# Performance work log

Hardware: AMD Instinct MI355X
Metric: run time of the kernel (lower is better)

The kernel has to match this reference:

```python
import jax, jax.numpy as jnp
import numpy as np
import math

EMBED_DIM = 768
NUM_FRAMES = 48
NUM_FREQS = 10
C_IN = 3
FOURIER_DIM = 4 * NUM_FREQS  # include_uv=False
PM_HID = C_IN * 9 * 4        # patch_mlp_ratio=4
OM_HID = EMBED_DIM * 4       # out_mlp_ratio=4
B, N, T, H, W = 4, 8192, 48, 256, 256


def setup_inputs() -> dict:
    key = jax.random.key(0)
    ks = jax.random.split(key, 16)
    uv = jax.random.uniform(ks[0], (B, N, 2), dtype=jnp.float32)
    ts = jax.random.randint(ks[1], (B, N, 3), 0, NUM_FRAMES).astype(jnp.float32)
    query = jnp.concatenate([uv, ts], axis=-1)  # (B,N,5)
    images = jax.random.normal(ks[2], (B, C_IN, T, H, W), dtype=jnp.float32)
    def xavier(k, fan_in, fan_out):
        lim = math.sqrt(6.0 / (fan_in + fan_out))
        return jax.random.uniform(k, (fan_in, fan_out), dtype=jnp.float32, minval=-lim, maxval=lim)
    return {
        "query": query,
        "images": images,
        "uv_w": xavier(ks[3], FOURIER_DIM, EMBED_DIM),
        "uv_b": jnp.zeros((EMBED_DIM,), jnp.float32),
        "t_src_emb": 0.02 * jax.random.normal(ks[4], (NUM_FRAMES, EMBED_DIM), dtype=jnp.float32),
        "t_tgt_emb": 0.02 * jax.random.normal(ks[5], (NUM_FRAMES, EMBED_DIM), dtype=jnp.float32),
        "t_cam_emb": 0.02 * jax.random.normal(ks[6], (NUM_FRAMES, EMBED_DIM), dtype=jnp.float32),
        "pm_w1": xavier(ks[7], C_IN * 9, PM_HID),
        "pm_b1": jnp.zeros((PM_HID,), jnp.float32),
        "pm_w2": xavier(ks[8], PM_HID, EMBED_DIM),
        "pm_b2": jnp.zeros((EMBED_DIM,), jnp.float32),
        "om_w1": xavier(ks[9], EMBED_DIM, OM_HID),
        "om_b1": jnp.zeros((OM_HID,), jnp.float32),
        "om_w2": xavier(ks[10], OM_HID, EMBED_DIM),
        "om_b2": jnp.zeros((EMBED_DIM,), jnp.float32),
    }


def reference(query, images, uv_w, uv_b, t_src_emb, t_tgt_emb, t_cam_emb,
              pm_w1, pm_b1, pm_w2, pm_b2, om_w1, om_b1, om_w2, om_b2):
    # images: (B,C,T,H,W) -> (B,T,C,H,W)
    images = jnp.transpose(images, (0, 2, 1, 3, 4))
    Bq, Nq, _ = query.shape
    _, Tq, C, Hh, Ww = images.shape

    uv = jnp.clip(query[..., 0:2].astype(jnp.float32), 0.0, 1.0)  # (B,N,2)
    t_src = jnp.clip(jnp.round(query[..., 2]).astype(jnp.int32), 0, NUM_FRAMES - 1)
    t_tgt = jnp.clip(jnp.round(query[..., 3]).astype(jnp.int32), 0, NUM_FRAMES - 1)
    t_cam = jnp.clip(jnp.round(query[..., 4]).astype(jnp.int32), 0, NUM_FRAMES - 1)

    # Fourier features of (u,v)
    fb = 2.0 ** jnp.arange(NUM_FREQS, dtype=jnp.float32)  # (F,)
    u = uv[..., 0:1]
    v = uv[..., 1:2]
    up = (2.0 * math.pi) * u * fb  # (B,N,F)
    vp = (2.0 * math.pi) * v * fb
    feat = jnp.concatenate([jnp.sin(up), jnp.cos(up), jnp.sin(vp), jnp.cos(vp)], axis=-1)

    token1 = feat @ uv_w + uv_b              # (B,N,D)
    token2 = t_src_emb[t_src]                # embedding lookups
    token3 = t_tgt_emb[t_tgt]
    token4 = t_cam_emb[t_cam]

    # 3x3 patch gather centered at discrete (u,v) pixel of frame t_src
    x = jnp.round(uv[..., 0] * (Ww - 1)).astype(jnp.int32)  # (B,N)
    y = jnp.round(uv[..., 1] * (Hh - 1)).astype(jnp.int32)
    d = jnp.arange(-1, 2, dtype=jnp.int32)
    x_idx = jnp.clip(x[..., None] + d, 0, Ww - 1)  # (B,N,3)
    y_idx = jnp.clip(y[..., None] + d, 0, Hh - 1)  # (B,N,3)
    b_idx = jnp.arange(Bq)[:, None, None, None, None]
    c_idx = jnp.arange(C)[:, None, None]
    # direct fancy-index gather -> (B,N,C,3,3); avoids materializing (B,N,C,H,W)
    patches = images[b_idx,
                     t_src[:, :, None, None, None],
                     c_idx,
                     y_idx[:, :, None, :, None],
                     x_idx[:, :, None, None, :]]
    patch_flat = patches.reshape(Bq, Nq, C * 9)

    h = jax.nn.gelu(patch_flat @ pm_w1 + pm_b1, approximate=False)
    token5 = h @ pm_w2 + pm_b2

    out = token1 + token2 + token3 + token4 + token5
    out = jax.nn.gelu(out @ om_w1 + om_b1, approximate=False) @ om_w2 + om_b2
    return out
```

## Files before the change

### kernel.cpp

```cpp
#include <hip/hip_runtime.h>

typedef __bf16 bf16x8 __attribute__((ext_vector_type(8)));
typedef float  f32x4  __attribute__((ext_vector_type(4)));

#define GAS(p) ((const __attribute__((address_space(1))) void*)(p))
#define LAS(p) ((__attribute__((address_space(3))) void*)(p))
#define VMCNT(n) asm volatile("s_waitcnt vmcnt(" #n ")" ::: "memory")

__device__ __forceinline__ float gelu_exact(float x) {
    return 0.5f * x * (1.f + erff(x * 0.70710678118654752440f));
}

enum { EPI_X = 0, EPI_GELU = 1, EPI_OUT = 2 };

__global__ __launch_bounds__(256) void stage1_kernel(
    const float* __restrict__ query, const float* __restrict__ images,
    const float* __restrict__ pm_w1, const float* __restrict__ pm_b1,
    __bf16* __restrict__ G, int* __restrict__ tbuf)
{
    __shared__ float patch[4][28];
    const int wave = threadIdx.x >> 6, lane = threadIdx.x & 63;
    const int p = blockIdx.x * 4 + wave;
    const float* q = query + (size_t)p * 5;
    float u = fminf(fmaxf(q[0], 0.f), 1.f);
    float v = fminf(fmaxf(q[1], 0.f), 1.f);
    int ts = min(max((int)rintf(q[2]), 0), 47);
    int tt = min(max((int)rintf(q[3]), 0), 47);
    int tc = min(max((int)rintf(q[4]), 0), 47);
    const int b = p >> 13;
    if (lane < 27) {
        int c = lane / 9, rem = lane % 9, dy = rem / 3, dx = rem % 3;
        int x = (int)rintf(u * 255.f), y = (int)rintf(v * 255.f);
        int xx = min(max(x + dx - 1, 0), 255);
        int yy = min(max(y + dy - 1, 0), 255);
        size_t idx = ((size_t)((b * 3 + c) * 48 + ts) << 16) + ((size_t)yy << 8) + (size_t)xx;
        patch[wave][lane] = images[idx];
    }
    if (lane < 40) {
        int i = lane % 10;
        float base = (lane < 20) ? u : v;
        float ph = 6.28318530717958647693f * base * exp2f((float)i);
        float val = ((lane / 10) & 1) ? cosf(ph) : sinf(ph);
        G[(size_t)p * 192 + lane] = (__bf16)val;
    }
    for (int j = 148 + lane; j < 192; j += 64) G[(size_t)p * 192 + j] = (__bf16)0.f;
    if (lane < 3) tbuf[p * 3 + lane] = (lane == 0) ? ts : (lane == 1) ? tt : tc;
    __syncthreads();
    for (int j = lane; j < 108; j += 64) {
        float acc = pm_b1[j];
        #pragma unroll
        for (int i2 = 0; i2 < 27; i2++)
            acc = fmaf(patch[wave][i2], pm_w1[i2 * 108 + j], acc);
        G[(size_t)p * 192 + 40 + j] = (__bf16)gelu_exact(acc);
    }
}

__global__ __launch_bounds__(256) void transpose_to_bf16(
    const float* __restrict__ src, __bf16* __restrict__ dst, int R, int C)
{
    __shared__ float t[32][33];
    const int c0 = blockIdx.x * 32, r0 = blockIdx.y * 32;
    const int tx = threadIdx.x & 31, ty = threadIdx.x >> 5;
    #pragma unroll
    for (int i = 0; i < 32; i += 8)
        t[ty + i][tx] = src[(size_t)(r0 + ty + i) * C + (c0 + tx)];
    __syncthreads();
    #pragma unroll
    for (int i = 0; i < 32; i += 8)
        dst[(size_t)(c0 + ty + i) * R + (r0 + tx)] = (__bf16)t[tx][ty + i];
}

__global__ __launch_bounds__(256) void build_wcat(
    const float* __restrict__ uv_w, const float* __restrict__ pm_w2, __bf16* __restrict__ Wt)
{
    int idx = blockIdx.x * 256 + threadIdx.x;
    int n = idx / 192, k = idx % 192;
    float v = 0.f;
    if (k < 40) v = uv_w[k * 768 + n];
    else if (k < 148) v = pm_w2[(k - 40) * 768 + n];
    Wt[idx] = (__bf16)v;
}

template <int EPI, typename OutT>
__global__ __launch_bounds__(256) void gemm_bt(
    const __bf16* __restrict__ A, const __bf16* __restrict__ Bt, int K,
    const float* __restrict__ bias, const float* __restrict__ bias2,
    const int* __restrict__ tbuf,
    const float* __restrict__ e0, const float* __restrict__ e1, const float* __restrict__ e2,
    OutT* __restrict__ Cmat, int N)
{
    __shared__ __attribute__((aligned(16))) __bf16 As[128 * 64];
    __shared__ __attribute__((aligned(16))) __bf16 Bs[128 * 64];
    const int tid = threadIdx.x;
    const int wave = tid >> 6, lane = tid & 63;
    const int wr = wave >> 1, wc = wave & 1;
    const int quad = lane >> 4, l15 = lane & 15;
    const int sw = l15 & 7;

    const int ntiles = N >> 7;
    const int per_super = ntiles << 3;
    const int id = blockIdx.x;
    const int sup = id / per_super, rem = id - sup * per_super;
    const long m0 = (long)(sup * 8 + (rem & 7)) << 7;
    const long n0 = (long)(rem >> 3) << 7;

    f32x4 acc[4][4];
    #pragma unroll
    for (int i = 0; i < 4; i++)
        #pragma unroll
        for (int j = 0; j < 4; j++)
            #pragma unroll
            for (int r = 0; r < 4; r++)
                acc[i][j][r] = 0.f;

    const __bf16* pa[4]; const __bf16* pb[4];
    __bf16* la[4]; __bf16* lb[4];
    #pragma unroll
    for (int t = 0; t < 4; t++) {
        int c = (t * 4 + wave) * 64 + lane;
        int row = c >> 3, s = c & 7, g = s ^ (row & 7);
        pa[t] = A  + (m0 + row) * (long)K + g * 8;
        pb[t] = Bt + (n0 + row) * (long)K + g * 8;
        la[t] = As + (t * 4 + wave) * 512;
        lb[t] = Bs + (t * 4 + wave) * 512;
    }

    for (int kt = 0; kt < K; kt += 64) {
        #pragma unroll
        for (int t = 0; t < 4; t++) {
            __builtin_amdgcn_global_load_lds(GAS(pa[t] + kt), LAS(la[t]), 16, 0, 0);
            __builtin_amdgcn_global_load_lds(GAS(pb[t] + kt), LAS(lb[t]), 16, 0, 0);
        }
        __syncthreads();
        #pragma unroll
        for (int h = 0; h < 2; h++) {
            const int slot = ((h * 4 + quad) ^ sw) * 8;
            bf16x8 af[4], bfv[4];
            #pragma unroll
            for (int i = 0; i < 4; i++)
                af[i] = *(const bf16x8*)&As[(wr * 64 + i * 16 + l15) * 64 + slot];
            #pragma unroll
            for (int j = 0; j < 4; j++)
                bfv[j] = *(const bf16x8*)&Bs[(wc * 64 + j * 16 + l15) * 64 + slot];
            #pragma unroll
            for (int i = 0; i < 4; i++)
                #pragma unroll
                for (int j = 0; j < 4; j++)
                    acc[i][j] = __builtin_amdgcn_mfma_f32_16x16x32_bf16(af[i], bfv[j], acc[i][j], 0, 0, 0);
        }
        __syncthreads();
    }

    #pragma unroll
    for (int i = 0; i < 4; i++) {
        #pragma unroll
        for (int r = 0; r < 4; r++) {
            long row = m0 + wr * 64 + i * 16 + quad * 4 + r;
            int t0 = 0, t1 = 0, t2 = 0;
            if constexpr (EPI == EPI_X) {
                t0 = tbuf[row * 3 + 0];
                t1 = tbuf[row * 3 + 1];
                t2 = tbuf[row * 3 + 2];
            }
            #pragma unroll
            for (int j = 0; j < 4; j++) {
                long col = n0 + wc * 64 + j * 16 + l15;
                float val = acc[i][j][r];
                if constexpr (EPI == EPI_X) {
                    val += bias[col] + bias2[col];
                    val += e0[t0 * 768 + col] + e1[t1 * 768 + col] + e2[t2 * 768 + col];
                    Cmat[row * (long)N + col] = (OutT)val;
                } else if constexpr (EPI == EPI_GELU) {
                    val += bias[col];
                    Cmat[row * (long)N + col] = (OutT)gelu_exact(val);
                } else {
                    val += bias[col];
                    Cmat[row * (long)N + col] = (OutT)val;
                }
            }
        }
    }
}

template <int EPI, typename OutT>
__global__ __launch_bounds__(512, 2) void gemm256(
    const __bf16* __restrict__ A, const __bf16* __restrict__ Bt, int K,
    const float* __restrict__ bias, OutT* __restrict__ Cmat, int N)
{
    extern __shared__ __attribute__((aligned(16))) __bf16 smem[];
    const int tid = threadIdx.x;
    const int wave = tid >> 6, lane = tid & 63;
    const int wr = wave >> 2, wc = wave & 3;
    const int quad = lane >> 4, l15 = lane & 15;

    const int ntiles = N >> 8;
    const int per_super = ntiles << 3;
    const int id = blockIdx.x;
    const int sup = id / per_super, rem = id - sup * per_super;
    const long m0 = (long)(sup * 8 + (rem & 7)) << 8;
    const long n0 = (long)(rem >> 3) << 8;

    f32x4 acc[8][4];
    #pragma unroll
    for (int i = 0; i < 8; i++)
        #pragma unroll
        for (int n = 0; n < 4; n++)
            #pragma unroll
            for (int r = 0; r < 4; r++)
                acc[i][n][r] = 0.f;

    const __bf16* srcA[2]; const __bf16* srcB[2];
    int ldsA[2], ldsB[2];
    #pragma unroll
    for (int i = 0; i < 2; i++) {
        int c = i * 512 + tid;
        int row = c >> 2, s = c & 3, g = s ^ ((row >> 1) & 3);
        srcA[i] = A  + (m0 + row) * (long)K + g * 8;
        srcB[i] = Bt + (n0 + row) * (long)K + g * 8;
        ldsA[i] = (i * 512 + wave * 64) * 8;
        ldsB[i] = (i * 512 + wave * 64) * 8;
    }

    auto stage = [&](int t) {
        const int buf = (t & 3) * 8192;
        const long koff = (long)t * 32;
        #pragma unroll
        for (int i = 0; i < 2; i++) {
            __builtin_amdgcn_global_load_lds(GAS(srcA[i] + koff), LAS(smem + buf + ldsA[i]), 16, 0, 0);
            __builtin_amdgcn_global_load_lds(GAS(srcB[i] + koff), LAS(smem + 32768 + buf + ldsB[i]), 16, 0, 0);
        }
    };

    const int slot = ((quad ^ ((l15 >> 1) & 3)) * 8);
    const int aoff = (wr * 128 + l15) * 32 + slot;
    const int boff = (wc * 64 + l15) * 32 + slot;

    auto compute = [&](int j) {
        const __bf16* ab = smem + (j & 3) * 8192 + aoff;
        const __bf16* bb = smem + 32768 + (j & 3) * 8192 + boff;
        bf16x8 af[8], bv[4];
        #pragma unroll
        for (int i = 0; i < 8; i++) af[i] = *(const bf16x8*)(ab + i * 512);
        #pragma unroll
        for (int n = 0; n < 4; n++) bv[n] = *(const bf16x8*)(bb + n * 512);
        __builtin_amdgcn_s_setprio(1);
        #pragma unroll
        for (int i = 0; i < 8; i++)
            #pragma unroll
            for (int n = 0; n < 4; n++)
                acc[i][n] = __builtin_amdgcn_mfma_f32_16x16x32_bf16(af[i], bv[n], acc[i][n], 0, 0, 0);
        __builtin_amdgcn_s_setprio(0);
        __builtin_amdgcn_sched_barrier(0);
    };

    const int nk = K >> 5;
    stage(0); stage(1); stage(2);
    for (int j = 0; j < nk - 3; ++j) {
        __builtin_amdgcn_s_barrier();
        stage(j + 3);
        VMCNT(12);
        __builtin_amdgcn_s_barrier();
        __builtin_amdgcn_sched_barrier(0);
        compute(j);
    }
    VMCNT(8);
    __builtin_amdgcn_s_barrier();
    __builtin_amdgcn_sched_barrier(0);
    compute(nk - 3);
    VMCNT(4);
    __builtin_amdgcn_s_barrier();
    __builtin_amdgcn_sched_barrier(0);
    compute(nk - 2);
    VMCNT(0);
    __builtin_amdgcn_s_barrier();
    __builtin_amdgcn_sched_barrier(0);
    compute(nk - 1);

    #pragma unroll
    for (int i = 0; i < 8; i++) {
        #pragma unroll
        for (int r = 0; r < 4; r++) {
            const long row = m0 + wr * 128 + i * 16 + quad * 4 + r;
            #pragma unroll
            for (int n = 0; n < 4; n++) {
                const long col = n0 + wc * 64 + n * 16 + l15;
                float val = acc[i][n][r] + bias[col];
                if constexpr (EPI == EPI_GELU)
                    Cmat[row * (long)N + col] = (OutT)gelu_exact(val);
                else
                    Cmat[row * (long)N + col] = (OutT)val;
            }
        }
    }
}

static constexpr size_t OFF_G  = 0;
static constexpr size_t OFF_T  = 12582912;
static constexpr size_t OFF_WC = 12976128;
static constexpr size_t OFF_W1 = 13271040;
static constexpr size_t OFF_W2 = 17989632;
static constexpr size_t OFF_X  = 22708224;
static constexpr size_t OFF_H2 = 73039872;

extern "C" void kernel_launch(void* const* d_in, const int* in_sizes, int n_in,
                              void* d_out, int out_size, void* d_ws, size_t ws_size,
                              hipStream_t stream)
{
    const float* query  = (const float*)d_in[0];
    const float* images = (const float*)d_in[1];
    const float* uv_w   = (const float*)d_in[2];
    const float* uv_b   = (const float*)d_in[3];
    const float* e_src  = (const float*)d_in[4];
    const float* e_tgt  = (const float*)d_in[5];
    const float* e_cam  = (const float*)d_in[6];
    const float* pm_w1  = (const float*)d_in[7];
    const float* pm_b1  = (const float*)d_in[8];
    const float* pm_w2  = (const float*)d_in[9];
    const float* pm_b2  = (const float*)d_in[10];
    const float* om_w1  = (const float*)d_in[11];
    const float* om_b1  = (const float*)d_in[12];
    const float* om_w2  = (const float*)d_in[13];
    const float* om_b2  = (const float*)d_in[14];
    float* out = (float*)d_out;
    char* ws = (char*)d_ws;

    __bf16* G    = (__bf16*)(ws + OFF_G);
    int*    tb   = (int*)(ws + OFF_T);
    __bf16* Wcat = (__bf16*)(ws + OFF_WC);
    __bf16* W1t  = (__bf16*)(ws + OFF_W1);
    __bf16* W2t  = (__bf16*)(ws + OFF_W2);
    __bf16* X    = (__bf16*)(ws + OFF_X);
    __bf16* H2   = (__bf16*)(ws + OFF_H2);

    static bool attr_done = false;
    if (!attr_done) {
        hipFuncSetAttribute(reinterpret_cast<const void*>(gemm256<EPI_GELU, __bf16>),
                            hipFuncAttributeMaxDynamicSharedMemorySize, 131072);
        hipFuncSetAttribute(reinterpret_cast<const void*>(gemm256<EPI_OUT, float>),
                            hipFuncAttributeMaxDynamicSharedMemorySize, 131072);
        attr_done = true;
    }

    stage1_kernel<<<8192, 256, 0, stream>>>(query, images, pm_w1, pm_b1, G, tb);
    transpose_to_bf16<<<dim3(3072 / 32, 768 / 32), 256, 0, stream>>>(om_w1, W1t, 768, 3072);
    transpose_to_bf16<<<dim3(768 / 32, 3072 / 32), 256, 0, stream>>>(om_w2, W2t, 3072, 768);
    build_wcat<<<576, 256, 0, stream>>>(uv_w, pm_w2, Wcat);

    gemm_bt<EPI_X, __bf16><<<256 * 6, 256, 0, stream>>>(
        G, Wcat, 192, uv_b, pm_b2, tb, e_src, e_tgt, e_cam, X, 768);

    long Mc = 1024;
    for (long cand = 32768; cand >= 1024; cand >>= 1)
        if (OFF_H2 + (size_t)cand * 3072 * 2 <= ws_size) { Mc = cand; break; }

    for (long m = 0; m < 32768; m += Mc) {
        gemm256<EPI_GELU, __bf16><<<(Mc / 256) * 12, 512, 131072, stream>>>(
            X + m * 768, W1t, 768, om_b1, H2, 3072);
        gemm256<EPI_OUT, float><<<(Mc / 256) * 3, 512, 131072, stream>>>(
            H2, W2t, 3072, om_b2, out + m * 768, 768);
    }
}
```

Baseline: 706.0 us.

## Restructure gemm256 main loop into fine-grained interleaved load/compute phases

Reworks the 256x256 bf16 GEMM pipeline from a 4-deep K=32 ring into double-buffered K=64 tiles, each split into four phases (two K-halves times two M-halves). Each phase issues one slice of the next global-to-LDS loads, then runs 16 MFMAs, so memory traffic is spread across compute and fewer fragment registers are live. It also drops the XOR swizzle on LDS addressing, which may bring back LDS bank conflicts. The extra barriers per phase add synchronisation overhead.

```diff
diff --git a/kernel.cpp b/kernel.cpp
--- a/kernel.cpp
+++ b/kernel.cpp
@@ -6,6 +6,7 @@
 #define GAS(p) ((const __attribute__((address_space(1))) void*)(p))
 #define LAS(p) ((__attribute__((address_space(3))) void*)(p))
 #define VMCNT(n) asm volatile("s_waitcnt vmcnt(" #n ")" ::: "memory")
+#define NOP_STMT ((void)0)
 
 __device__ __forceinline__ float gelu_exact(float x) {
     return 0.5f * x * (1.f + erff(x * 0.70710678118654752440f));
@@ -182,12 +183,62 @@
     }
 }
 
+#define PHASE(bufc, khc, mhc, STAGE_STMT, WAIT_STMT) do {                     \
+    const __bf16* _ab = As + ((bufc) * 2 + (khc)) * 8192 +                    \
+                        (wr * 128 + (mhc) * 64 + l15) * 32 + quad * 8;        \
+    bf16x8 af[4];                                                             \
+    af[0] = *(const bf16x8*)(_ab);                                            \
+    af[1] = *(const bf16x8*)(_ab + 512);                                      \
+    af[2] = *(const bf16x8*)(_ab + 1024);                                     \
+    af[3] = *(const bf16x8*)(_ab + 1536);                                     \
+    if ((mhc) == 0) {                                                         \
+        const __bf16* _bb = Bs + ((bufc) * 2 + (khc)) * 8192 +                \
+                            (wc * 64 + l15) * 32 + quad * 8;                  \
+        bv[0] = *(const bf16x8*)(_bb);                                        \
+        bv[1] = *(const bf16x8*)(_bb + 512);                                  \
+        bv[2] = *(const bf16x8*)(_bb + 1024);                                 \
+        bv[3] = *(const bf16x8*)(_bb + 1536);                                 \
+    }                                                                         \
+    STAGE_STMT;                                                               \
+    WAIT_STMT;                                                                \
+    __builtin_amdgcn_sched_barrier(0);                                        \
+    __builtin_amdgcn_s_barrier();                                             \
+    asm volatile("s_waitcnt lgkmcnt(0)" ::: "memory");                        \
+    __builtin_amdgcn_sched_barrier(0);                                        \
+    __builtin_amdgcn_s_setprio(1);                                            \
+    _Pragma("unroll")                                                         \
+    for (int _ii = 0; _ii < 4; _ii++)                                         \
+        _Pragma("unroll")                                                     \
+        for (int _n = 0; _n < 4; _n++)                                        \
+            acc[(mhc) * 4 + _ii][_n] = __builtin_amdgcn_mfma_f32_16x16x32_bf16( \
+                af[_ii], bv[_n], acc[(mhc) * 4 + _ii][_n], 0, 0, 0);          \
+    __builtin_amdgcn_s_setprio(0);                                            \
+    __builtin_amdgcn_sched_barrier(0);                                        \
+    __builtin_amdgcn_s_barrier();                                             \
+} while (0)
+
+#define STAGE_A(buf, kh, t) do {                                              \
+    __bf16* _d = As + ((buf) * 2 + (kh)) * 8192;                              \
+    const long _ko = (long)(t) * 64 + (kh) * 32;                              \
+    __builtin_amdgcn_global_load_lds(GAS(aSrc0 + _ko), LAS(_d + ldsOff0), 16, 0, 0); \
+    __builtin_amdgcn_global_load_lds(GAS(aSrc1 + _ko), LAS(_d + ldsOff1), 16, 0, 0); \
+} while (0)
+
+#define STAGE_B(buf, kh, t) do {                                              \
+    __bf16* _d = Bs + ((buf) * 2 + (kh)) * 8192;                              \
+    const long _ko = (long)(t) * 64 + (kh) * 32;                              \
+    __builtin_amdgcn_global_load_lds(GAS(bSrc0 + _ko), LAS(_d + ldsOff0), 16, 0, 0); \
+    __builtin_amdgcn_global_load_lds(GAS(bSrc1 + _ko), LAS(_d + ldsOff1), 16, 0, 0); \
+} while (0)
+
 template <int EPI, typename OutT>
 __global__ __launch_bounds__(512, 2) void gemm256(
     const __bf16* __restrict__ A, const __bf16* __restrict__ Bt, int K,
     const float* __restrict__ bias, OutT* __restrict__ Cmat, int N)
 {
     extern __shared__ __attribute__((aligned(16))) __bf16 smem[];
+    __bf16* As = smem;
+    __bf16* Bs = smem + 32768;
     const int tid = threadIdx.x;
     const int wave = tid >> 6, lane = tid & 63;
     const int wr = wave >> 2, wc = wave & 3;
@@ -209,72 +260,44 @@
             for (int r = 0; r < 4; r++)
                 acc[i][n][r] = 0.f;
 
-    const __bf16* srcA[2]; const __bf16* srcB[2];
-    int ldsA[2], ldsB[2];
-    #pragma unroll
-    for (int i = 0; i < 2; i++) {
-        int c = i * 512 + tid;
-        int row = c >> 2, s = c & 3, g = s ^ ((row >> 1) & 3);
-        srcA[i] = A  + (m0 + row) * (long)K + g * 8;
-        srcB[i] = Bt + (n0 + row) * (long)K + g * 8;
-        ldsA[i] = (i * 512 + wave * 64) * 8;
-        ldsB[i] = (i * 512 + wave * 64) * 8;
-    }
-
-    auto stage = [&](int t) {
-        const int buf = (t & 3) * 8192;
-        const long koff = (long)t * 32;
-        #pragma unroll
-        for (int i = 0; i < 2; i++) {
-            __builtin_amdgcn_global_load_lds(GAS(srcA[i] + koff), LAS(smem + buf + ldsA[i]), 16, 0, 0);
-            __builtin_amdgcn_global_load_lds(GAS(srcB[i] + koff), LAS(smem + 32768 + buf + ldsB[i]), 16, 0, 0);
-        }
-    };
-
-    const int slot = ((quad ^ ((l15 >> 1) & 3)) * 8);
-    const int aoff = (wr * 128 + l15) * 32 + slot;
-    const int boff = (wc * 64 + l15) * 32 + slot;
-
-    auto compute = [&](int j) {
-        const __bf16* ab = smem + (j & 3) * 8192 + aoff;
-        const __bf16* bb = smem + 32768 + (j & 3) * 8192 + boff;
-        bf16x8 af[8], bv[4];
-        #pragma unroll
-        for (int i = 0; i < 8; i++) af[i] = *(const bf16x8*)(ab + i * 512);
-        #pragma unroll
-        for (int n = 0; n < 4; n++) bv[n] = *(const bf16x8*)(bb + n * 512);
-        __builtin_amdgcn_s_setprio(1);
-        #pragma unroll
-        for (int i = 0; i < 8; i++)
-            #pragma unroll
-            for (int n = 0; n < 4; n++)
-                acc[i][n] = __builtin_amdgcn_mfma_f32_16x16x32_bf16(af[i], bv[n], acc[i][n], 0, 0, 0);
-        __builtin_amdgcn_s_setprio(0);
-        __builtin_amdgcn_sched_barrier(0);
-    };
-
-    const int nk = K >> 5;
-    stage(0); stage(1); stage(2);
-    for (int j = 0; j < nk - 3; ++j) {
-        __builtin_amdgcn_s_barrier();
-        stage(j + 3);
-        VMCNT(12);
-        __builtin_amdgcn_s_barrier();
-        __builtin_amdgcn_sched_barrier(0);
-        compute(j);
-    }
-    VMCNT(8);
-    __builtin_amdgcn_s_barrier();
-    __builtin_amdgcn_sched_barrier(0);
-    compute(nk - 3);
+    const int row0 = tid >> 2, row1 = (512 + tid) >> 2;
+    const int c0 = (tid & 3) * 8, c1 = ((512 + tid) & 3) * 8;
+    const __bf16* aSrc0 = A  + (m0 + row0) * (long)K + c0;
+    const __bf16* aSrc1 = A  + (m0 + row1) * (long)K + c1;
+    const __bf16* bSrc0 = Bt + (n0 + row0) * (long)K + c0;
+    const __bf16* bSrc1 = Bt + (n0 + row1) * (long)K + c1;
+    const int ldsOff0 = wave * 512;
+    const int ldsOff1 = 4096 + wave * 512;
+
+    const int nk = K >> 6;
+    STAGE_A(0, 0, 0); STAGE_B(0, 0, 0);
+    STAGE_A(0, 1, 0); STAGE_B(0, 1, 0);
+    STAGE_A(1, 0, 1); STAGE_B(1, 0, 1);
     VMCNT(4);
     __builtin_amdgcn_s_barrier();
-    __builtin_amdgcn_sched_barrier(0);
-    compute(nk - 2);
-    VMCNT(0);
-    __builtin_amdgcn_s_barrier();
-    __builtin_amdgcn_sched_barrier(0);
-    compute(nk - 1);
+
+    bf16x8 bv[4];
+    for (int t = 0; t < nk - 2; ++t) {
+        const int b = t & 1;
+        PHASE(b, 0, 0, STAGE_A(b ^ 1, 1, t + 1), NOP_STMT);
+        PHASE(b, 0, 1, STAGE_B(b ^ 1, 1, t + 1), NOP_STMT);
+        PHASE(b, 1, 0, STAGE_A(b, 0, t + 2), NOP_STMT);
+        PHASE(b, 1, 1, STAGE_B(b, 0, t + 2), VMCNT(4));
+    }
+    {
+        const int b = (nk - 2) & 1;
+        PHASE(b, 0, 0, STAGE_A(b ^ 1, 1, nk - 1), NOP_STMT);
+        PHASE(b, 0, 1, STAGE_B(b ^ 1, 1, nk - 1), NOP_STMT);
+        PHASE(b, 1, 0, NOP_STMT, NOP_STMT);
+        PHASE(b, 1, 1, NOP_STMT, VMCNT(0));
+    }
+    {
+        const int b = (nk - 1) & 1;
+        PHASE(b, 0, 0, NOP_STMT, NOP_STMT);
+        PHASE(b, 0, 1, NOP_STMT, NOP_STMT);
+        PHASE(b, 1, 0, NOP_STMT, NOP_STMT);
+        PHASE(b, 1, 1, NOP_STMT, NOP_STMT);
+    }
 
     #pragma unroll
     for (int i = 0; i < 8; i++) {
```

Result: faster. 692.1 us (-2.0%).

## Load GEMM A operand directly to registers, stage only B through LDS

Applied to the files above, without the earlier changes.

The main 256x256 GEMM no longer stages the A tile through shared memory. Each lane loads its A fragments straight from global memory into registers, prefetching one K-step ahead. Only B goes through LDS, in a double-buffered, half-K ping-pong schedule, which halves LDS to 64KB per block and removes A's LDS write/read traffic. In exchange, A is read with uncoalesced 16-byte row-strided global loads, may be fetched redundantly across the four column waves, and the pipeline is shallower with more barriers per K step.

```diff
diff --git a/kernel.cpp b/kernel.cpp
--- a/kernel.cpp
+++ b/kernel.cpp
@@ -182,16 +182,33 @@
     }
 }
 
+#define MFMA32(AF, BV)                                                        \
+    _Pragma("unroll")                                                         \
+    for (int _i = 0; _i < 8; _i++)                                            \
+        _Pragma("unroll")                                                     \
+        for (int _n = 0; _n < 4; _n++)                                        \
+            acc[_i][_n] = __builtin_amdgcn_mfma_f32_16x16x32_bf16(            \
+                AF[_i], BV[_n], acc[_i][_n], 0, 0, 0);
+
+#define STAGE_BH(bufp, khp, tp) do {                                          \
+    __bf16* _d = Bs + ((bufp) * 2 + (khp)) * 8192;                            \
+    const long _ko = (long)(tp) * 64 + (khp) * 32;                            \
+    __builtin_amdgcn_global_load_lds(GAS(bSrc0 + _ko), LAS(_d + ldsOff0), 16, 0, 0); \
+    __builtin_amdgcn_global_load_lds(GAS(bSrc1 + _ko), LAS(_d + ldsOff1), 16, 0, 0); \
+} while (0)
+
 template <int EPI, typename OutT>
 __global__ __launch_bounds__(512, 2) void gemm256(
     const __bf16* __restrict__ A, const __bf16* __restrict__ Bt, int K,
     const float* __restrict__ bias, OutT* __restrict__ Cmat, int N)
 {
-    extern __shared__ __attribute__((aligned(16))) __bf16 smem[];
+    extern __shared__ __attribute__((aligned(16))) __bf16 Bs[];
     const int tid = threadIdx.x;
     const int wave = tid >> 6, lane = tid & 63;
     const int wr = wave >> 2, wc = wave & 3;
     const int quad = lane >> 4, l15 = lane & 15;
+    const int swsl = (quad ^ ((l15 >> 1) & 3)) * 8;
+    const int bboff = (wc * 64 + l15) * 32 + swsl;
 
     const int ntiles = N >> 8;
     const int per_super = ntiles << 3;
@@ -209,72 +226,64 @@
             for (int r = 0; r < 4; r++)
                 acc[i][n][r] = 0.f;
 
-    const __bf16* srcA[2]; const __bf16* srcB[2];
-    int ldsA[2], ldsB[2];
-    #pragma unroll
-    for (int i = 0; i < 2; i++) {
-        int c = i * 512 + tid;
-        int row = c >> 2, s = c & 3, g = s ^ ((row >> 1) & 3);
-        srcA[i] = A  + (m0 + row) * (long)K + g * 8;
-        srcB[i] = Bt + (n0 + row) * (long)K + g * 8;
-        ldsA[i] = (i * 512 + wave * 64) * 8;
-        ldsB[i] = (i * 512 + wave * 64) * 8;
-    }
-
-    auto stage = [&](int t) {
-        const int buf = (t & 3) * 8192;
-        const long koff = (long)t * 32;
-        #pragma unroll
-        for (int i = 0; i < 2; i++) {
-            __builtin_amdgcn_global_load_lds(GAS(srcA[i] + koff), LAS(smem + buf + ldsA[i]), 16, 0, 0);
-            __builtin_amdgcn_global_load_lds(GAS(srcB[i] + koff), LAS(smem + 32768 + buf + ldsB[i]), 16, 0, 0);
-        }
-    };
-
-    const int slot = ((quad ^ ((l15 >> 1) & 3)) * 8);
-    const int aoff = (wr * 128 + l15) * 32 + slot;
-    const int boff = (wc * 64 + l15) * 32 + slot;
-
-    auto compute = [&](int j) {
-        const __bf16* ab = smem + (j & 3) * 8192 + aoff;
-        const __bf16* bb = smem + 32768 + (j & 3) * 8192 + boff;
-        bf16x8 af[8], bv[4];
-        #pragma unroll
-        for (int i = 0; i < 8; i++) af[i] = *(const bf16x8*)(ab + i * 512);
-        #pragma unroll
-        for (int n = 0; n < 4; n++) bv[n] = *(const bf16x8*)(bb + n * 512);
+    const __bf16* aRow[8];
+    #pragma unroll
+    for (int i = 0; i < 8; i++)
+        aRow[i] = A + (m0 + wr * 128 + i * 16 + l15) * (long)K + quad * 8;
+
+    const int row0 = tid >> 2, row1 = (512 + tid) >> 2;
+    const int g0 = (tid & 3) ^ ((row0 >> 1) & 3);
+    const int g1 = ((512 + tid) & 3) ^ ((row1 >> 1) & 3);
+    const __bf16* bSrc0 = Bt + (n0 + row0) * (long)K + g0 * 8;
+    const __bf16* bSrc1 = Bt + (n0 + row1) * (long)K + g1 * 8;
+    const int ldsOff0 = wave * 512, ldsOff1 = 4096 + wave * 512;
+
+    const int nt = K >> 6;
+
+    STAGE_BH(0, 0, 0); STAGE_BH(0, 1, 0); STAGE_BH(1, 0, 1);
+    bf16x8 afA[8], afB[8], bv[4];
+    #pragma unroll
+    for (int i = 0; i < 8; i++) afA[i] = *(const bf16x8*)(aRow[i]);
+    VMCNT(0);
+    __builtin_amdgcn_s_barrier();
+
+    for (int t = 0; t < nt; ++t) {
+        const int b = t & 1;
+        VMCNT(2);
+        {
+            const __bf16* bb = Bs + (b * 2 + 0) * 8192 + bboff;
+            #pragma unroll
+            for (int n = 0; n < 4; n++) bv[n] = *(const bf16x8*)(bb + n * 512);
+        }
+        #pragma unroll
+        for (int i = 0; i < 8; i++) afB[i] = *(const bf16x8*)(aRow[i] + t * 64 + 32);
+        __builtin_amdgcn_s_barrier();
+        asm volatile("s_waitcnt lgkmcnt(0)" ::: "memory");
+        __builtin_amdgcn_sched_barrier(0);
         __builtin_amdgcn_s_setprio(1);
-        #pragma unroll
-        for (int i = 0; i < 8; i++)
-            #pragma unroll
-            for (int n = 0; n < 4; n++)
-                acc[i][n] = __builtin_amdgcn_mfma_f32_16x16x32_bf16(af[i], bv[n], acc[i][n], 0, 0, 0);
+        MFMA32(afA, bv);
         __builtin_amdgcn_s_setprio(0);
         __builtin_amdgcn_sched_barrier(0);
-    };
-
-    const int nk = K >> 5;
-    stage(0); stage(1); stage(2);
-    for (int j = 0; j < nk - 3; ++j) {
+        if (t + 1 < nt) STAGE_BH((t + 1) & 1, 1, t + 1);
+        VMCNT(2);
+        {
+            const __bf16* bb = Bs + (b * 2 + 1) * 8192 + bboff;
+            #pragma unroll
+            for (int n = 0; n < 4; n++) bv[n] = *(const bf16x8*)(bb + n * 512);
+        }
+        if (t + 1 < nt) {
+            #pragma unroll
+            for (int i = 0; i < 8; i++) afA[i] = *(const bf16x8*)(aRow[i] + (t + 1) * 64);
+        }
         __builtin_amdgcn_s_barrier();
-        stage(j + 3);
-        VMCNT(12);
-        __builtin_amdgcn_s_barrier();
+        asm volatile("s_waitcnt lgkmcnt(0)" ::: "memory");
         __builtin_amdgcn_sched_barrier(0);
-        compute(j);
-    }
-    VMCNT(8);
-    __builtin_amdgcn_s_barrier();
-    __builtin_amdgcn_sched_barrier(0);
-    compute(nk - 3);
-    VMCNT(4);
-    __builtin_amdgcn_s_barrier();
-    __builtin_amdgcn_sched_barrier(0);
-    compute(nk - 2);
-    VMCNT(0);
-    __builtin_amdgcn_s_barrier();
-    __builtin_amdgcn_sched_barrier(0);
-    compute(nk - 1);
+        __builtin_amdgcn_s_setprio(1);
+        MFMA32(afB, bv);
+        __builtin_amdgcn_s_setprio(0);
+        __builtin_amdgcn_sched_barrier(0);
+        if (t + 2 < nt) STAGE_BH(b, 0, t + 2);
+    }
 
     #pragma unroll
     for (int i = 0; i < 8; i++) {
@@ -335,9 +344,9 @@
     static bool attr_done = false;
     if (!attr_done) {
         hipFuncSetAttribute(reinterpret_cast<const void*>(gemm256<EPI_GELU, __bf16>),
-                            hipFuncAttributeMaxDynamicSharedMemorySize, 131072);
+                            hipFuncAttributeMaxDynamicSharedMemorySize, 65536);
         hipFuncSetAttribute(reinterpret_cast<const void*>(gemm256<EPI_OUT, float>),
-                            hipFuncAttributeMaxDynamicSharedMemorySize, 131072);
+                            hipFuncAttributeMaxDynamicSharedMemorySize, 65536);
         attr_done = true;
     }
 
@@ -354,9 +363,9 @@
         if (OFF_H2 + (size_t)cand * 3072 * 2 <= ws_size) { Mc = cand; break; }
 
     for (long m = 0; m < 32768; m += Mc) {
-        gemm256<EPI_GELU, __bf16><<<(Mc / 256) * 12, 512, 131072, stream>>>(
+        gemm256<EPI_GELU, __bf16><<<(Mc / 256) * 12, 512, 65536, stream>>>(
             X + m * 768, W1t, 768, om_b1, H2, 3072);
-        gemm256<EPI_OUT, float><<<(Mc / 256) * 3, 512, 131072, stream>>>(
+        gemm256<EPI_OUT, float><<<(Mc / 256) * 3, 512, 65536, stream>>>(
             H2, W2t, 3072, om_b2, out + m * 768, 768);
     }
 }
```

Measured after the change: 1.061 ms. 50.3% more time.
